# Optimization experiments

Measured on AMD Instinct MI355X. Metric: run time of the kernel, lower is better.

## Reference

```python
import jax, jax.numpy as jnp
import numpy as np

BLOCK = 8

def _dct_matrix(n: int) -> np.ndarray:
    # Orthonormal DCT-II basis: D[k, m] = s_k * cos(pi*(2m+1)*k/(2n))
    k = np.arange(n)[:, None].astype(np.float64)
    m = np.arange(n)[None, :].astype(np.float64)
    D = np.cos(np.pi * (2.0 * m + 1.0) * k / (2.0 * n))
    D *= np.sqrt(2.0 / n)
    D[0, :] *= np.sqrt(0.5)
    return D.astype(np.float32)


def setup_inputs() -> dict:
    key = jax.random.key(0)
    x = jax.random.normal(key, (32, 3, 512, 512), dtype=jnp.float32)
    return {"x": x}


def reference(x):
    B, C, H, W = x.shape
    D = jnp.asarray(_dct_matrix(BLOCK))  # [8, 8]
    Hb, Wb = H // BLOCK, W // BLOCK
    # [B, C, Hb, 8, Wb, 8]
    blocks = x.reshape(B, C, Hb, BLOCK, Wb, BLOCK)
    # Per-block 2D DCT-II (ortho): out = D @ block @ D^T
    out = jnp.einsum('ij,lk,bcHjWk->bcHiWl', D, D, blocks)
    return out.reshape(B, C, H, W)
```

## Files before the change

### kernel.cpp

```cpp
#include <hip/hip_runtime.h>

#define A1 0.4903926402f
#define A3 0.4157348061f
#define A5 0.2777851165f
#define A7 0.0975451610f
#define B2 0.4619397663f
#define B6 0.1913417162f
#define C4 0.3535533906f

__device__ __constant__ float Dc[8][8] = {
    { C4,  C4,  C4,  C4,  C4,  C4,  C4,  C4},
    { A1,  A3,  A5,  A7, -A7, -A5, -A3, -A1},
    { B2,  B6, -B6, -B2, -B2, -B6,  B6,  B2},
    { A3, -A7, -A1, -A5,  A5,  A1,  A7, -A3},
    { C4, -C4, -C4,  C4,  C4, -C4, -C4,  C4},
    { A5, -A1,  A7,  A3, -A3, -A7,  A1, -A5},
    { B6, -B2,  B2, -B6, -B6,  B2, -B2,  B6},
    { A7, -A5,  A3, -A1,  A1, -A3,  A5, -A7},
};

#define IMG_W 512

__global__ __launch_bounds__(256) void dct8x8_kernel(const float* __restrict__ x,
                                                     float* __restrict__ y,
                                                     int total_blocks) {
    int t = blockIdx.x * blockDim.x + threadIdx.x;
    if (t >= total_blocks) return;

    int plane = t >> 12;
    int blk   = t & 4095;
    int br    = blk >> 6;
    int bc    = blk & 63;

    const size_t base = (size_t)plane * (IMG_W * IMG_W)
                      + (size_t)br * 8 * IMG_W
                      + (size_t)bc * 8;
    const float* __restrict__ src = x + base;
    float*       __restrict__ dst = y + base;

    float X[8][8];
#pragma unroll
    for (int r = 0; r < 8; ++r) {
        float4 a = *reinterpret_cast<const float4*>(src + r * IMG_W);
        float4 b = *reinterpret_cast<const float4*>(src + r * IMG_W + 4);
        X[r][0] = a.x; X[r][1] = a.y; X[r][2] = a.z; X[r][3] = a.w;
        X[r][4] = b.x; X[r][5] = b.y; X[r][6] = b.z; X[r][7] = b.w;
    }

    float T[8][8];
#pragma unroll
    for (int i = 0; i < 8; ++i) {
#pragma unroll
        for (int k = 0; k < 8; ++k) {
            float s = 0.0f;
#pragma unroll
            for (int j = 0; j < 8; ++j) s = fmaf(Dc[i][j], X[j][k], s);
            T[i][k] = s;
        }
    }

#pragma unroll
    for (int i = 0; i < 8; ++i) {
        float o[8];
#pragma unroll
        for (int l = 0; l < 8; ++l) {
            float s = 0.0f;
#pragma unroll
            for (int k = 0; k < 8; ++k) s = fmaf(T[i][k], Dc[l][k], s);
            o[l] = s;
        }
        float4 a = {o[0], o[1], o[2], o[3]};
        float4 b = {o[4], o[5], o[6], o[7]};
        *reinterpret_cast<float4*>(dst + i * IMG_W)     = a;
        *reinterpret_cast<float4*>(dst + i * IMG_W + 4) = b;
    }
}

extern "C" void kernel_launch(void* const* d_in, const int* in_sizes, int n_in,
                              void* d_out, int out_size, void* d_ws, size_t ws_size,
                              hipStream_t stream) {
    const float* x = (const float*)d_in[0];
    float* y = (float*)d_out;

    const int total_blocks = out_size / 64;
    const int threads = 256;
    const int grid = (total_blocks + threads - 1) / threads;

    dct8x8_kernel<<<grid, threads, 0, stream>>>(x, y, total_blocks);
}
```

Measured before the change: 41.54 us.

## Split each 8x8 DCT block across eight threads with LDS transposes

Instead of one thread computing a whole 8x8 block with 64 live registers, each thread now handles one row of a block. It does the row transform, transposes through padded shared memory, does the column transform, then transposes back before a coalesced float4 store. Each workgroup covers a 256-pixel-wide strip of 32 blocks. This cuts register pressure, so occupancy can rise to eight workgroups per CU, and it makes global loads contiguous across a wavefront. The cost is three barriers and extra LDS traffic per block.

```diff
diff --git a/kernel.cpp b/kernel.cpp
--- a/kernel.cpp
+++ b/kernel.cpp
@@ -20,60 +20,69 @@
 };
 
 #define IMG_W 512
+#define LDS_FLOATS (8 * 32 * 9)
 
-__global__ __launch_bounds__(256) void dct8x8_kernel(const float* __restrict__ x,
-                                                     float* __restrict__ y,
-                                                     int total_blocks) {
-    int t = blockIdx.x * blockDim.x + threadIdx.x;
-    if (t >= total_blocks) return;
+__global__ __launch_bounds__(256, 8) void dct8x8_kernel(const float* __restrict__ x,
+                                                        float* __restrict__ y) {
+    __shared__ float lds[LDS_FLOATS];
 
-    int plane = t >> 12;
-    int blk   = t & 4095;
-    int br    = blk >> 6;
-    int bc    = blk & 63;
+    const int t   = threadIdx.x;
+    const int blk = t & 31;
+    const int r8  = t >> 5;
+
+    const int wg    = blockIdx.x;
+    const int plane = wg >> 7;
+    const int rem   = wg & 127;
+    const int ty    = rem >> 1;
+    const int tx    = rem & 1;
 
     const size_t base = (size_t)plane * (IMG_W * IMG_W)
-                      + (size_t)br * 8 * IMG_W
-                      + (size_t)bc * 8;
-    const float* __restrict__ src = x + base;
-    float*       __restrict__ dst = y + base;
+                      + (size_t)ty * 8 * IMG_W
+                      + (size_t)tx * 256
+                      + (size_t)blk * 8;
 
-    float X[8][8];
+    const float* __restrict__ src = x + base + (size_t)r8 * IMG_W;
+    float4 a = *reinterpret_cast<const float4*>(src);
+    float4 b = *reinterpret_cast<const float4*>(src + 4);
+    float xv[8] = {a.x, a.y, a.z, a.w, b.x, b.y, b.z, b.w};
+
 #pragma unroll
-    for (int r = 0; r < 8; ++r) {
-        float4 a = *reinterpret_cast<const float4*>(src + r * IMG_W);
-        float4 b = *reinterpret_cast<const float4*>(src + r * IMG_W + 4);
-        X[r][0] = a.x; X[r][1] = a.y; X[r][2] = a.z; X[r][3] = a.w;
-        X[r][4] = b.x; X[r][5] = b.y; X[r][6] = b.z; X[r][7] = b.w;
+    for (int c = 0; c < 8; ++c) {
+        float s = 0.0f;
+#pragma unroll
+        for (int m = 0; m < 8; ++m) s = fmaf(Dc[c][m], xv[m], s);
+        lds[(c * 32 + blk) * 9 + r8] = s;
     }
+    __syncthreads();
 
-    float T[8][8];
+    const int c = r8;
+    float z[8];
+#pragma unroll
+    for (int r = 0; r < 8; ++r) z[r] = lds[(c * 32 + blk) * 9 + r];
+
+    float w[8];
 #pragma unroll
     for (int i = 0; i < 8; ++i) {
+        float s = 0.0f;
 #pragma unroll
-        for (int k = 0; k < 8; ++k) {
-            float s = 0.0f;
-#pragma unroll
-            for (int j = 0; j < 8; ++j) s = fmaf(Dc[i][j], X[j][k], s);
-            T[i][k] = s;
-        }
+        for (int r = 0; r < 8; ++r) s = fmaf(Dc[i][r], z[r], s);
+        w[i] = s;
     }
+    __syncthreads();
 
 #pragma unroll
-    for (int i = 0; i < 8; ++i) {
-        float o[8];
+    for (int i = 0; i < 8; ++i) lds[(i * 32 + blk) * 9 + c] = w[i];
+    __syncthreads();
+
+    float o[8];
 #pragma unroll
-        for (int l = 0; l < 8; ++l) {
-            float s = 0.0f;
-#pragma unroll
-            for (int k = 0; k < 8; ++k) s = fmaf(T[i][k], Dc[l][k], s);
-            o[l] = s;
-        }
-        float4 a = {o[0], o[1], o[2], o[3]};
-        float4 b = {o[4], o[5], o[6], o[7]};
-        *reinterpret_cast<float4*>(dst + i * IMG_W)     = a;
-        *reinterpret_cast<float4*>(dst + i * IMG_W + 4) = b;
-    }
+    for (int cc = 0; cc < 8; ++cc) o[cc] = lds[(r8 * 32 + blk) * 9 + cc];
+
+    float* __restrict__ dst = y + base + (size_t)r8 * IMG_W;
+    float4 oa = {o[0], o[1], o[2], o[3]};
+    float4 ob = {o[4], o[5], o[6], o[7]};
+    *reinterpret_cast<float4*>(dst)     = oa;
+    *reinterpret_cast<float4*>(dst + 4) = ob;
 }
 
 extern "C" void kernel_launch(void* const* d_in, const int* in_sizes, int n_in,
@@ -82,9 +91,7 @@
     const float* x = (const float*)d_in[0];
     float* y = (float*)d_out;
 
-    const int total_blocks = out_size / 64;
-    const int threads = 256;
-    const int grid = (total_blocks + threads - 1) / threads;
+    const int grid = out_size / 2048;
 
-    dct8x8_kernel<<<grid, threads, 0, stream>>>(x, y, total_blocks);
+    dct8x8_kernel<<<grid, 256, 0, stream>>>(x, y);
 }
```

New measurement: 39.00 us. -6.1%, faster.

## Split each 8x8 DCT block across two lanes with shuffle exchange

Applied to the files above, without the earlier changes.

Each 8x8 block is now handled by two adjacent threads, each owning four columns. Each thread computes the column transform on its half and exchanges intermediates with its partner via __shfl_xor for the row transform. The DCT matrix moves from __constant__ memory to compile-time constants, and outputs use nontemporal stores. This doubles thread count and halves per-thread registers to improve occupancy and latency hiding, at the cost of shuffle traffic and narrower per-thread loads.

```diff
diff --git a/kernel.cpp b/kernel.cpp
--- a/kernel.cpp
+++ b/kernel.cpp
@@ -1,4 +1,6 @@
 #include <hip/hip_runtime.h>
+
+typedef float v4f __attribute__((ext_vector_type(4)));
 
 #define A1 0.4903926402f
 #define A3 0.4157348061f
@@ -8,71 +10,90 @@
 #define B6 0.1913417162f
 #define C4 0.3535533906f
 
-__device__ __constant__ float Dc[8][8] = {
-    { C4,  C4,  C4,  C4,  C4,  C4,  C4,  C4},
-    { A1,  A3,  A5,  A7, -A7, -A5, -A3, -A1},
-    { B2,  B6, -B6, -B2, -B2, -B6,  B6,  B2},
-    { A3, -A7, -A1, -A5,  A5,  A1,  A7, -A3},
-    { C4, -C4, -C4,  C4,  C4, -C4, -C4,  C4},
-    { A5, -A1,  A7,  A3, -A3, -A7,  A1, -A5},
-    { B6, -B2,  B2, -B6, -B6,  B2, -B2,  B6},
-    { A7, -A5,  A3, -A1,  A1, -A3,  A5, -A7},
-};
-
 #define IMG_W 512
 
 __global__ __launch_bounds__(256) void dct8x8_kernel(const float* __restrict__ x,
                                                      float* __restrict__ y,
-                                                     int total_blocks) {
-    int t = blockIdx.x * blockDim.x + threadIdx.x;
-    if (t >= total_blocks) return;
+                                                     int nhalf) {
+    constexpr float D[8][8] = {
+        { C4,  C4,  C4,  C4,  C4,  C4,  C4,  C4},
+        { A1,  A3,  A5,  A7, -A7, -A5, -A3, -A1},
+        { B2,  B6, -B6, -B2, -B2, -B6,  B6,  B2},
+        { A3, -A7, -A1, -A5,  A5,  A1,  A7, -A3},
+        { C4, -C4, -C4,  C4,  C4, -C4, -C4,  C4},
+        { A5, -A1,  A7,  A3, -A3, -A7,  A1, -A5},
+        { B6, -B2,  B2, -B6, -B6,  B2, -B2,  B6},
+        { A7, -A5,  A3, -A1,  A1, -A3,  A5, -A7},
+    };
 
-    int plane = t >> 12;
-    int blk   = t & 4095;
-    int br    = blk >> 6;
-    int bc    = blk & 63;
+    const int t = blockIdx.x * 256 + threadIdx.x;
+    if (t >= nhalf) return;
+
+    const int h = t & 1;
+    const int g = t >> 1;
+    const int plane = g >> 12;
+    const int b     = g & 4095;
+    const int br    = b >> 6;
+    const int bc    = b & 63;
 
     const size_t base = (size_t)plane * (IMG_W * IMG_W)
                       + (size_t)br * 8 * IMG_W
-                      + (size_t)bc * 8;
+                      + (size_t)bc * 8 + (size_t)h * 4;
+
     const float* __restrict__ src = x + base;
-    float*       __restrict__ dst = y + base;
-
-    float X[8][8];
+    float X[8][4];
 #pragma unroll
     for (int r = 0; r < 8; ++r) {
-        float4 a = *reinterpret_cast<const float4*>(src + r * IMG_W);
-        float4 b = *reinterpret_cast<const float4*>(src + r * IMG_W + 4);
-        X[r][0] = a.x; X[r][1] = a.y; X[r][2] = a.z; X[r][3] = a.w;
-        X[r][4] = b.x; X[r][5] = b.y; X[r][6] = b.z; X[r][7] = b.w;
+        v4f v = *reinterpret_cast<const v4f*>(src + (size_t)r * IMG_W);
+        X[r][0] = v.x; X[r][1] = v.y; X[r][2] = v.z; X[r][3] = v.w;
     }
 
-    float T[8][8];
+    float Dh[4][8];
+#pragma unroll
+    for (int jj = 0; jj < 4; ++jj)
+#pragma unroll
+        for (int m = 0; m < 8; ++m)
+            Dh[jj][m] = h ? D[4 + jj][m] : D[jj][m];
+
+    float T[8][4];
+#pragma unroll
+    for (int i = 0; i < 8; ++i)
+#pragma unroll
+        for (int k = 0; k < 4; ++k) {
+            float s = 0.0f;
+#pragma unroll
+            for (int r = 0; r < 8; ++r) s = fmaf(D[i][r], X[r][k], s);
+            T[i][k] = s;
+        }
+
+    float* __restrict__ dst = y + base;
 #pragma unroll
     for (int i = 0; i < 8; ++i) {
+        float r4[4];
 #pragma unroll
-        for (int k = 0; k < 8; ++k) {
+        for (int kk = 0; kk < 4; ++kk) r4[kk] = __shfl_xor(T[i][kk], 1, 64);
+
+        float lo[4], hi[4];
+#pragma unroll
+        for (int kk = 0; kk < 4; ++kk) {
+            lo[kk] = h ? r4[kk]   : T[i][kk];
+            hi[kk] = h ? T[i][kk] : r4[kk];
+        }
+
+        float ov[4];
+#pragma unroll
+        for (int jj = 0; jj < 4; ++jj) {
             float s = 0.0f;
 #pragma unroll
-            for (int j = 0; j < 8; ++j) s = fmaf(Dc[i][j], X[j][k], s);
-            T[i][k] = s;
+            for (int k = 0; k < 4; ++k) s = fmaf(lo[k], Dh[jj][k],     s);
+#pragma unroll
+            for (int k = 0; k < 4; ++k) s = fmaf(hi[k], Dh[jj][4 + k], s);
+            ov[jj] = s;
         }
-    }
 
-#pragma unroll
-    for (int i = 0; i < 8; ++i) {
-        float o[8];
-#pragma unroll
-        for (int l = 0; l < 8; ++l) {
-            float s = 0.0f;
-#pragma unroll
-            for (int k = 0; k < 8; ++k) s = fmaf(T[i][k], Dc[l][k], s);
-            o[l] = s;
-        }
-        float4 a = {o[0], o[1], o[2], o[3]};
-        float4 b = {o[4], o[5], o[6], o[7]};
-        *reinterpret_cast<float4*>(dst + i * IMG_W)     = a;
-        *reinterpret_cast<float4*>(dst + i * IMG_W + 4) = b;
+        v4f o;
+        o.x = ov[0]; o.y = ov[1]; o.z = ov[2]; o.w = ov[3];
+        __builtin_nontemporal_store(o, reinterpret_cast<v4f*>(dst + (size_t)i * IMG_W));
     }
 }
 
@@ -82,9 +103,8 @@
     const float* x = (const float*)d_in[0];
     float* y = (float*)d_out;
 
-    const int total_blocks = out_size / 64;
-    const int threads = 256;
-    const int grid = (total_blocks + threads - 1) / threads;
+    const int nhalf = out_size / 32;
+    const int grid  = (nhalf + 255) / 256;
 
-    dct8x8_kernel<<<grid, threads, 0, stream>>>(x, y, total_blocks);
+    dct8x8_kernel<<<grid, 256, 0, stream>>>(x, y, nhalf);
 }
```

Measured after the change: 34.86 us. -16.1%, faster.
